# Kernel tuning notes

Measured on AMD Instinct MI355X. Metric: run time of the kernel, lower is better.

The kernel has to match this reference:

```python
import jax, jax.numpy as jnp
import numpy as np

B, N, C, H = 16, 512, 128, 8
T, DEG = B * N, 32
E = T * DEG
EQ = 8            # mul of 0e and of 1o in output irreps
EQD = EQ + 3 * EQ # 32 = irreps_out.dim
RW = 64           # radial MLP width
AVG_NEIGH = 10.0


def setup_inputs() -> dict:
    key = jax.random.key(0)
    ks = jax.random.split(key, 24)
    X = jax.random.normal(ks[0], (B, N, C), jnp.float32)
    adj_mask = jnp.ones((B, H, N, N), bool)
    edge_index = jax.random.randint(ks[1], (2, E), 0, T)
    edge_vectors = jax.random.normal(ks[2], (E, 3), jnp.float32)
    batch_mapping = jnp.repeat(jnp.arange(B), N)  # uniform, sorted
    nrm = lambda k, s, fan: jax.random.normal(k, s, jnp.float32) / np.sqrt(fan)
    p = dict(
        # SAB (set-transformer MAB(X,X)) params
        Wq=nrm(ks[3], (C, C), C), bq=jnp.zeros((C,)),
        Wk=nrm(ks[4], (C, C), C), bk=jnp.zeros((C,)),
        Wv=nrm(ks[5], (C, C), C), bv=jnp.zeros((C,)),
        Wf=nrm(ks[6], (C, C), C), bf=jnp.zeros((C,)),
        g0=jnp.ones((C,)), b0=jnp.zeros((C,)),
        g1=jnp.ones((C,)), b1=jnp.zeros((C,)),
        # cross connection inv->equiv (nn.Linear)
        Wc=nrm(ks[7], (C, C), C), bc=jnp.zeros((C,)),
        # e3nn-style weights (std-1; fan-in normalization applied in forward)
        W1=jax.random.normal(ks[8], (C, C), jnp.float32),        # linear_1 on 0e feats
        Wr0=jax.random.normal(ks[9], (1, RW), jnp.float32),      # radial MLP
        Wr1=jax.random.normal(ks[10], (RW, RW), jnp.float32),
        Wr2=jax.random.normal(ks[11], (RW, 2 * C), jnp.float32),  # 2 tp paths x C channels
        W20=jax.random.normal(ks[12], (C, EQ), jnp.float32),     # linear_2, 0e block
        W21=jax.random.normal(ks[13], (C, EQ), jnp.float32),     # linear_2, 1o block
        Wsc=jax.random.normal(ks[14], (C, EQ), jnp.float32),     # self-connection (0e only)
        # equiv->scalar and gate (nn.Linear on irreps_out.dim=32)
        Wes=nrm(ks[15], (EQD, C), EQD), bes=jnp.zeros((C,)),
        Wg=nrm(ks[16], (EQD, C), EQD), bg=jnp.zeros((C,)),
    )
    return dict(X=X, adj_mask=adj_mask, edge_index=edge_index,
                edge_vectors=edge_vectors, batch_mapping=batch_mapping, **p)


def _ln(x, g, b):
    mu = jnp.mean(x, -1, keepdims=True)
    var = jnp.var(x, -1, keepdims=True)
    return (x - mu) * jax.lax.rsqrt(var + 1e-5) * g + b


def _sab(X, adj_mask, Wq, bq, Wk, bk, Wv, bv, Wf, bf, g0, b0, g1, b1):
    b, n, d = X.shape
    dh = d // H
    q = (X @ Wq + bq).reshape(b, n, H, dh).transpose(0, 2, 1, 3)
    k = (X @ Wk + bk).reshape(b, n, H, dh).transpose(0, 2, 1, 3)
    v = (X @ Wv + bv).reshape(b, n, H, dh).transpose(0, 2, 1, 3)
    s = jnp.einsum('bhqd,bhkd->bhqk', q, k) / np.sqrt(dh)
    s = jnp.where(adj_mask, s, jnp.float32(-1e9))
    a = jax.nn.softmax(s, -1)
    o = q + jnp.einsum('bhqk,bhkd->bhqd', a, v)
    o = o.transpose(0, 2, 1, 3).reshape(b, n, d)
    o = _ln(o, g0, b0)
    o = o + jax.nn.relu(o @ Wf + bf)
    return _ln(o, g1, b1)


def _dense_sparse_idx(batch_mapping):
    counts = jax.ops.segment_sum(jnp.ones_like(batch_mapping), batch_mapping, B)
    offs = jnp.concatenate([jnp.zeros((1,), counts.dtype), jnp.cumsum(counts)[:-1]])
    pos = jnp.arange(batch_mapping.shape[0]) - offs[batch_mapping]
    return pos


def reference(X, adj_mask, edge_index, edge_vectors, batch_mapping,
              Wq, bq, Wk, bk, Wv, bv, Wf, bf, g0, b0, g1, b1,
              Wc, bc, W1, Wr0, Wr1, Wr2, W20, W21, Wsc, Wes, bes, Wg, bg):
    inv = _sab(X, adj_mask, Wq, bq, Wk, bk, Wv, bv, Wf, bf, g0, b0, g1, b1)

    pos = _dense_sparse_idx(batch_mapping)
    x_sp = X[batch_mapping, pos]                         # [T,C] dense->sparse
    xe = x_sp @ Wc + bc                                  # inv_to_equiv
    x1 = xe @ W1 / np.sqrt(C)                            # linear_1 (0e)

    # spherical harmonics (normalize=True, component norm); e3nn order (y,z,x)
    r = edge_vectors / jnp.clip(jnp.linalg.norm(edge_vectors, axis=-1, keepdims=True), 1e-12)
    Y1 = np.sqrt(3.0) * r[:, jnp.array([1, 2, 0])]       # [E,3]; Y0 == 1

    # radial MLP on edge_embedding == 1 (FullyConnectedNet, silu, fan-in norm)
    emb = jnp.ones((edge_index.shape[1], 1), X.dtype)
    h = jax.nn.silu(emb @ Wr0)
    h = jax.nn.silu(h @ Wr1 / np.sqrt(RW))
    w = h @ Wr2 / np.sqrt(RW)                            # [E, 2C]
    w0, w1 = w[:, :C], w[:, C:]

    snd, rcv = edge_index[0], edge_index[1]
    xs = x1[snd]                                         # gather [E,C]
    m0 = w0 * xs                                         # 0e x 0e -> 0e (Y0 = 1)
    m1 = (w1 * xs)[:, :, None] * Y1[:, None, :]          # 0e x 1o -> 1o [E,C,3]
    inv_sqrt = 1.0 / np.sqrt(AVG_NEIGH)
    a0 = jax.ops.segment_sum(m0, rcv, T) * inv_sqrt      # scatter-sum [T,C]
    a1 = jax.ops.segment_sum(m1.reshape(-1, C * 3), rcv, T).reshape(T, C, 3) * inv_sqrt

    out0 = a0 @ W20 / np.sqrt(C)                         # linear_2 per irrep
    out1 = jnp.einsum('tcm,ck->tkm', a1, W21) / np.sqrt(C)
    out0 = out0 + x_sp @ Wsc / np.sqrt(C)                # self-connection (node_attrs=1)
    eq = jnp.concatenate([out0, out1.reshape(T, 3 * EQ)], -1)  # [T,32]

    eq_scalar = eq @ Wes + bes
    gate = eq @ Wg + bg
    eq_dense = jnp.zeros_like(inv).at[batch_mapping, pos].set(eq_scalar)
    gate_dense = jnp.zeros_like(inv).at[batch_mapping, pos].set(gate)

    inv = inv * jax.nn.sigmoid(gate_dense)
    return inv + eq_dense
```

## Files before the change

kernel.cpp:

```cpp
#include <hip/hip_runtime.h>
#include <hip/hip_bf16.h>

#define BB 16
#define NN 512
#define CC 128
#define HH 8
#define DHD 16
#define TT 8192
#define EE 262144
#define RWD 64

__global__ void k_diag(float* __restrict__ out, int n, float code)
{
    int i = blockIdx.x*256 + threadIdx.x;
    if (i < n) out[i] = (i == 0) ? code : 0.f;
}

__global__ __launch_bounds__(512) void k_qkv(const float* __restrict__ X,
    const float* __restrict__ Wq, const float* __restrict__ bq,
    const float* __restrict__ Wk, const float* __restrict__ bk,
    const float* __restrict__ Wv, const float* __restrict__ bv,
    float* __restrict__ qb, float* __restrict__ kb, float* __restrict__ vb,
    int* __restrict__ counts)
{
    __shared__ float a_lds[128][17];
    const int tid  = threadIdx.x;
    const int row0 = blockIdx.x * 16;

    {
        int gid = blockIdx.x*512 + tid;
        if (gid < TT/4) ((int4*)counts)[gid] = make_int4(0,0,0,0);
    }

    const float4* X4 = (const float4*)(X + (size_t)row0*128);
    {
        int r = tid >> 5, k4 = (tid & 31) << 2;
        float4 v = X4[(r*128 + k4) >> 2];
        a_lds[k4+0][r] = v.x; a_lds[k4+1][r] = v.y;
        a_lds[k4+2][r] = v.z; a_lds[k4+3][r] = v.w;
    }
    __syncthreads();

    const int c  = tid & 127;
    const int q4 = tid >> 7;
    const float* Ws[3]  = {Wq, Wk, Wv};
    const float* bsx[3] = {bq, bk, bv};
    float* outs[3] = {qb, kb, vb};

    #pragma unroll
    for (int m = 0; m < 3; m++) {
        float acc[4];
        #pragma unroll
        for (int i = 0; i < 4; i++) acc[i] = 0.f;
        const float* bp = Ws[m] + c;
        for (int k = 0; k < 128; k++) {
            float b = bp[k*128];
            const float* ap = &a_lds[k][q4*4];
            #pragma unroll
            for (int i = 0; i < 4; i++) acc[i] = fmaf(ap[i], b, acc[i]);
        }
        float bia = bsx[m][c];
        float* op = outs[m];
        #pragma unroll
        for (int i = 0; i < 4; i++) {
            int r = row0 + q4*4 + i;
            int b_ = r >> 9, n_ = r & 511, h_ = c >> 4, d_ = c & 15;
            op[(((size_t)(b_*HH + h_)*NN + n_)*DHD) + d_] = acc[i] + bia;
        }
    }
}

__global__ __launch_bounds__(512) void k_attn(const float* __restrict__ qb,
                                              const float* __restrict__ kb,
                                              const float* __restrict__ vb,
                                              float* __restrict__ attn)
{
    __shared__ float k_lds[8192];
    __shared__ float v_lds[8192];
    int bh   = blockIdx.x >> 2;
    int tile = blockIdx.x & 3;
    const float4* kp = (const float4*)(kb + (size_t)bh*8192);
    const float4* vp = (const float4*)(vb + (size_t)bh*8192);
    float4* kl4 = (float4*)k_lds;
    float4* vl4 = (float4*)v_lds;
    for (int i = threadIdx.x; i < 2048; i += 512) {
        float4 kv = kp[i];
        kv.x *= 0.25f; kv.y *= 0.25f; kv.z *= 0.25f; kv.w *= 0.25f;
        kl4[i] = kv;
        vl4[i] = vp[i];
    }

    int r  = threadIdx.x & 127;
    int jq = threadIdx.x >> 7;
    int n  = tile*128 + r;
    float q[16];
    const float4* qp = (const float4*)(qb + ((size_t)bh*512 + n)*16);
    #pragma unroll
    for (int i = 0; i < 4; i++) {
        float4 v = qp[i];
        q[i*4+0] = v.x; q[i*4+1] = v.y; q[i*4+2] = v.z; q[i*4+3] = v.w;
    }
    __syncthreads();

    float l = 0.f, o[16];
    #pragma unroll
    for (int d = 0; d < 16; d++) o[d] = 0.f;

    int j0base = jq*128;
    for (int j0 = j0base; j0 < j0base + 128; j0 += 16) {
        float s[16];
        #pragma unroll
        for (int jj = 0; jj < 16; jj++) {
            const float* kr = &k_lds[(j0 + jj)*16];
            float a = 0.f;
            #pragma unroll
            for (int d = 0; d < 16; d++) a = fmaf(q[d], kr[d], a);
            s[jj] = a;
        }
        #pragma unroll
        for (int jj = 0; jj < 16; jj++) {
            float p = __expf(s[jj]);
            l += p;
            const float* vr = &v_lds[(j0 + jj)*16];
            #pragma unroll
            for (int d = 0; d < 16; d++) o[d] = fmaf(p, vr[d], o[d]);
        }
    }
    __syncthreads();
    float* scr = k_lds;
    if (jq > 0) {
        int base = ((jq-1)*128 + r)*18;
        scr[base + 0] = l;
        #pragma unroll
        for (int d = 0; d < 16; d++) scr[base + 1 + d] = o[d];
    }
    __syncthreads();
    if (jq == 0) {
        const float* s1 = &scr[((size_t)0*128 + r)*18];
        const float* s2 = &scr[((size_t)1*128 + r)*18];
        const float* s3 = &scr[((size_t)2*128 + r)*18];
        float L = l + s1[0] + s2[0] + s3[0];
        float invl = 1.f / L;
        int b_ = bh >> 3, h_ = bh & 7;
        float4* op = (float4*)(attn + ((size_t)(b_*512 + n))*128 + h_*16);
        #pragma unroll
        for (int i = 0; i < 4; i++) {
            float4 v;
            v.x = q[i*4+0] + (o[i*4+0] + s1[1+i*4+0] + s2[1+i*4+0] + s3[1+i*4+0])*invl;
            v.y = q[i*4+1] + (o[i*4+1] + s1[1+i*4+1] + s2[1+i*4+1] + s3[1+i*4+1])*invl;
            v.z = q[i*4+2] + (o[i*4+2] + s1[1+i*4+2] + s2[1+i*4+2] + s3[1+i*4+2])*invl;
            v.w = q[i*4+3] + (o[i*4+3] + s1[1+i*4+3] + s2[1+i*4+3] + s3[1+i*4+3])*invl;
            op[i] = v;
        }
    }
}

__global__ __launch_bounds__(512) void k_ffln(const float* __restrict__ A,
                                              const float* __restrict__ g0,
                                              const float* __restrict__ b0,
                                              const float* __restrict__ Wf,
                                              const float* __restrict__ bfp,
                                              const float* __restrict__ g1,
                                              const float* __restrict__ b1,
                                              float* __restrict__ out)
{
    __shared__ float a_lds[128][36];
    __shared__ float y_lds[32][129];
    __shared__ float red[32][16][2];
    __shared__ float mu_s[32], rs_s[32];
    const int tid  = threadIdx.x;
    const int row0 = blockIdx.x * 32;

    const float4* A4 = (const float4*)(A + (size_t)row0*128);
    for (int fid = tid; fid < 1024; fid += 512) {
        int r = fid >> 5, k4 = (fid & 31) << 2;
        float4 v = A4[(r*128 + k4) >> 2];
        a_lds[k4+0][r] = v.x; a_lds[k4+1][r] = v.y;
        a_lds[k4+2][r] = v.z; a_lds[k4+3][r] = v.w;
    }
    __syncthreads();

    int rr = tid >> 4, seg = tid & 15;
    {
        float s1 = 0.f, s2 = 0.f;
        #pragma unroll
        for (int i = 0; i < 8; i++) {
            float v = a_lds[seg*8 + i][rr];
            s1 += v; s2 += v*v;
        }
        red[rr][seg][0] = s1; red[rr][seg][1] = s2;
    }
    __syncthreads();
    if (seg == 0) {
        float a1 = 0.f, a2 = 0.f;
        #pragma unroll
        for (int s = 0; s < 16; s++) { a1 += red[rr][s][0]; a2 += red[rr][s][1]; }
        float mu = a1 * (1.f/128.f);
        float var = fmaxf(a2 * (1.f/128.f) - mu*mu, 0.f);
        mu_s[rr] = mu; rs_s[rr] = rsqrtf(var + 1e-5f);
    }
    __syncthreads();
    {
        float mu = mu_s[rr], rs = rs_s[rr];
        #pragma unroll
        for (int i = 0; i < 8; i++) {
            int k = seg*8 + i;
            float v = a_lds[k][rr];
            a_lds[k][rr] = (v - mu)*rs*g0[k] + b0[k];
        }
    }
    __syncthreads();

    const int c  = tid & 127;
    const int q4 = tid >> 7;
    float acc[8];
    #pragma unroll
    for (int i = 0; i < 8; i++) acc[i] = 0.f;
    const float* bp = Wf + c;
    for (int k = 0; k < 128; k++) {
        float b = bp[k*128];
        const float* ap = &a_lds[k][q4*8];
        #pragma unroll
        for (int i = 0; i < 8; i++) acc[i] = fmaf(ap[i], b, acc[i]);
    }
    float bia = bfp[c];
    #pragma unroll
    for (int i = 0; i < 8; i++) {
        int rl = q4*8 + i;
        float oln = a_lds[c][rl];
        y_lds[rl][c] = oln + fmaxf(acc[i] + bia, 0.f);
    }
    __syncthreads();

    {
        float s1 = 0.f, s2 = 0.f;
        #pragma unroll
        for (int i = 0; i < 8; i++) {
            float v = y_lds[rr][seg*8 + i];
            s1 += v; s2 += v*v;
        }
        red[rr][seg][0] = s1; red[rr][seg][1] = s2;
    }
    __syncthreads();
    if (seg == 0) {
        float a1 = 0.f, a2 = 0.f;
        #pragma unroll
        for (int s = 0; s < 16; s++) { a1 += red[rr][s][0]; a2 += red[rr][s][1]; }
        float mu = a1 * (1.f/128.f);
        float var = fmaxf(a2 * (1.f/128.f) - mu*mu, 0.f);
        mu_s[rr] = mu; rs_s[rr] = rsqrtf(var + 1e-5f);
    }
    __syncthreads();
    float g = g1[c], bb = b1[c];
    #pragma unroll
    for (int i = 0; i < 8; i++) {
        int rl = q4*8 + i;
        float v = y_lds[rl][c];
        out[(size_t)(row0 + rl)*128 + c] = (v - mu_s[rl])*rs_s[rl]*g + bb;
    }
}

__global__ __launch_bounds__(256) void k_zeq(const float* __restrict__ X,
    const float* __restrict__ Wr0, const float* __restrict__ Wr1,
    const float* __restrict__ Wr2,
    const float* __restrict__ Wc,  const float* __restrict__ W1,
    const float* __restrict__ bc,
    const float* __restrict__ W20, const float* __restrict__ W21,
    const float* __restrict__ Wsc,
    float* __restrict__ z, float* __restrict__ eqsc)
{
    const float SCALE_Z = 0.027950849718747372f;
    const float SC      = 0.08838834764831845f;
    __shared__ float a_lds[128][36];
    __shared__ float w_lds[128*24];
    __shared__ float wz[128][16];
    __shared__ float Pl[128][16];
    __shared__ float wsm[256];
    __shared__ float h0[RWD], h1[RWD];
    __shared__ float be[24];
    int tid = threadIdx.x;
    int row0 = blockIdx.x * 32;

    const float4* X4 = (const float4*)(X + (size_t)row0*128);
    for (int fid = tid; fid < 1024; fid += 256) {
        int r = fid >> 5, k4 = (fid & 31) << 2;
        float4 v = X4[(r*128 + k4) >> 2];
        a_lds[k4+0][r] = v.x; a_lds[k4+1][r] = v.y;
        a_lds[k4+2][r] = v.z; a_lds[k4+3][r] = v.w;
    }
    if (tid < RWD) { float x = Wr0[tid]; h0[tid] = x / (1.f + __expf(-x)); }
    __syncthreads();
    if (tid < RWD) {
        float s = 0.f;
        for (int i = 0; i < RWD; i++) s += h0[i] * Wr1[i*RWD + tid];
        s *= 0.125f;
        h1[tid] = s / (1.f + __expf(-s));
    }
    __syncthreads();
    {
        float s = 0.f;
        for (int i = 0; i < RWD; i++) s += h1[i] * Wr2[i*2*CC + tid];
        wsm[tid] = s * 0.125f;
    }
    __syncthreads();
    for (int idx = tid; idx < 2048; idx += 256) {
        int c = idx >> 4, j = idx & 15;
        wz[c][j] = (j < 8) ? W20[c*8 + j]*wsm[c] : W21[c*8 + (j-8)]*wsm[128 + c];
    }
    __syncthreads();
    {
        int d = tid >> 1, hf = tid & 1;
        float acc[8];
        #pragma unroll
        for (int jj = 0; jj < 8; jj++) acc[jj] = 0.f;
        const float4* wrow = (const float4*)(W1 + (size_t)d*128);
        for (int c4 = 0; c4 < 32; c4++) {
            float4 wv = wrow[c4];
            const float* z0 = &wz[c4*4 + 0][hf*8];
            const float* z1 = &wz[c4*4 + 1][hf*8];
            const float* z2 = &wz[c4*4 + 2][hf*8];
            const float* z3 = &wz[c4*4 + 3][hf*8];
            #pragma unroll
            for (int jj = 0; jj < 8; jj++) {
                float a = acc[jj];
                a = fmaf(wv.x, z0[jj], a);
                a = fmaf(wv.y, z1[jj], a);
                a = fmaf(wv.z, z2[jj], a);
                a = fmaf(wv.w, z3[jj], a);
                acc[jj] = a;
            }
        }
        #pragma unroll
        for (int jj = 0; jj < 8; jj++) Pl[d][hf*8 + jj] = acc[jj];
    }
    __syncthreads();
    {
        int i = tid >> 1, hf = tid & 1;
        float acc[8];
        #pragma unroll
        for (int jj = 0; jj < 8; jj++) acc[jj] = 0.f;
        const float4* crow = (const float4*)(Wc + (size_t)i*128);
        for (int d4 = 0; d4 < 32; d4++) {
            float4 wv = crow[d4];
            const float* p0 = &Pl[d4*4 + 0][hf*8];
            const float* p1 = &Pl[d4*4 + 1][hf*8];
            const float* p2 = &Pl[d4*4 + 2][hf*8];
            const float* p3 = &Pl[d4*4 + 3][hf*8];
            #pragma unroll
            for (int jj = 0; jj < 8; jj++) {
                float a = acc[jj];
                a = fmaf(wv.x, p0[jj], a);
                a = fmaf(wv.y, p1[jj], a);
                a = fmaf(wv.z, p2[jj], a);
                a = fmaf(wv.w, p3[jj], a);
                acc[jj] = a;
            }
        }
        const float SCZ = SC*SCALE_Z;
        #pragma unroll
        for (int jj = 0; jj < 8; jj++) w_lds[i*24 + hf*8 + jj] = acc[jj]*SCZ;
    }
    for (int idx = tid; idx < 1024; idx += 256) {
        int i = idx >> 3, j = idx & 7;
        w_lds[i*24 + 16 + j] = Wsc[i*8 + j]*SC;
    }
    if (tid < 24) {
        float a = 0.f;
        if (tid < 16) {
            for (int d = 0; d < 128; d++) a = fmaf(bc[d], Pl[d][tid], a);
            a *= SC*SCALE_Z;
        }
        be[tid] = a;
    }
    __syncthreads();

    int r = tid >> 3, seg = tid & 7;
    float a0 = be[seg], a1 = be[seg+8], a2 = 0.f;
    for (int k = 0; k < 128; k++) {
        float xv = a_lds[k][r];
        a0 = fmaf(xv, w_lds[k*24 + seg],      a0);
        a1 = fmaf(xv, w_lds[k*24 + seg + 8],  a1);
        a2 = fmaf(xv, w_lds[k*24 + seg + 16], a2);
    }
    size_t t = row0 + r;
    z[t*16 + seg]     = a0;
    z[t*16 + seg + 8] = a1;
    eqsc[t*8 + seg]   = a2;
}

__global__ void k_edge(const int* __restrict__ ei, const float* __restrict__ ev,
                       int* __restrict__ counts, int2* __restrict__ bucket,
                       float* __restrict__ y1)
{
    int e = blockIdx.x*256 + threadIdx.x;
    float x = ev[e*3], y = ev[e*3+1], zz = ev[e*3+2];
    float nrm = sqrtf(x*x + y*y + zz*zz);
    float inv = 1.f / fmaxf(nrm, 1e-12f);
    const float s3 = 1.7320508075688772f;
    y1[e*3 + 0] = s3 * y  * inv;
    y1[e*3 + 1] = s3 * zz * inv;
    y1[e*3 + 2] = s3 * x  * inv;
    int s = ei[e]      & (TT-1);
    int t = ei[EE + e] & (TT-1);
    int pos = atomicAdd(&counts[t], 1);
    if (pos < 128) bucket[(size_t)t*128 + pos] = make_int2(s, e);
}

__global__ __launch_bounds__(256) void k_gfin(const int* __restrict__ counts,
                                              const int2* __restrict__ bucket,
                                              const float* __restrict__ z,
                                              const float* __restrict__ y1,
                                              const float* __restrict__ eqsc,
                                              const float* __restrict__ inv,
                                              const float* __restrict__ Wes,
                                              const float* __restrict__ bes,
                                              const float* __restrict__ Wg,
                                              const float* __restrict__ bg,
                                              float* __restrict__ out)
{
    __shared__ float eql[8][33];
    int tid = threadIdx.x;
    int tb  = blockIdx.x*8;
    int tg  = tid >> 5;
    int t   = tb + tg;
    int j   = tid & 31;
    int deg = counts[t]; if (deg > 128) deg = 128; if (deg < 0) deg = 0;
    const int2* bk = bucket + (size_t)t*128;
    int jj = j - 8;
    int kk = jj / 3;
    int mm = jj - kk*3;
    int zi = (j < 8) ? j : (8 + kk);
    int mi = (j < 8) ? 0 : mm;
    bool isz = (j < 8);

    float ac0 = isz ? eqsc[(size_t)t*8 + j] : 0.f;
    float ac1 = 0.f, ac2 = 0.f, ac3 = 0.f;
    int p = 0;
    for (; p + 8 <= deg; p += 8) {
        int2 e0 = bk[p+0], e1 = bk[p+1], e2 = bk[p+2], e3 = bk[p+3];
        int2 e4 = bk[p+4], e5 = bk[p+5], e6 = bk[p+6], e7 = bk[p+7];
        float z0 = z[(size_t)e0.x*16 + zi], w0 = y1[(size_t)e0.y*3 + mi];
        float z1 = z[(size_t)e1.x*16 + zi], w1 = y1[(size_t)e1.y*3 + mi];
        float z2 = z[(size_t)e2.x*16 + zi], w2 = y1[(size_t)e2.y*3 + mi];
        float z3 = z[(size_t)e3.x*16 + zi], w3 = y1[(size_t)e3.y*3 + mi];
        float z4 = z[(size_t)e4.x*16 + zi], w4 = y1[(size_t)e4.y*3 + mi];
        float z5 = z[(size_t)e5.x*16 + zi], w5 = y1[(size_t)e5.y*3 + mi];
        float z6 = z[(size_t)e6.x*16 + zi], w6 = y1[(size_t)e6.y*3 + mi];
        float z7 = z[(size_t)e7.x*16 + zi], w7 = y1[(size_t)e7.y*3 + mi];
        ac0 = fmaf(z0, isz ? 1.f : w0, ac0);
        ac1 = fmaf(z1, isz ? 1.f : w1, ac1);
        ac2 = fmaf(z2, isz ? 1.f : w2, ac2);
        ac3 = fmaf(z3, isz ? 1.f : w3, ac3);
        ac0 = fmaf(z4, isz ? 1.f : w4, ac0);
        ac1 = fmaf(z5, isz ? 1.f : w5, ac1);
        ac2 = fmaf(z6, isz ? 1.f : w6, ac2);
        ac3 = fmaf(z7, isz ? 1.f : w7, ac3);
    }
    for (; p < deg; p++) {
        int2 se = bk[p];
        float v  = z[(size_t)se.x*16 + zi];
        float wv = y1[(size_t)se.y*3 + mi];
        ac0 = fmaf(v, isz ? 1.f : wv, ac0);
    }
    eql[tg][j] = (ac0 + ac1) + (ac2 + ac3);
    __syncthreads();

    int c = tid & 127, hf = tid >> 7;
    float aes[4], ag[4];
    float bse = bes[c], bgg = bg[c];
    #pragma unroll
    for (int r2 = 0; r2 < 4; r2++) { aes[r2] = bse; ag[r2] = bgg; }
    for (int jx = 0; jx < 32; jx++) {
        float we = Wes[jx*128 + c];
        float wg = Wg [jx*128 + c];
        #pragma unroll
        for (int r2 = 0; r2 < 4; r2++) {
            float v = eql[hf*4 + r2][jx];
            aes[r2] = fmaf(v, we, aes[r2]);
            ag[r2]  = fmaf(v, wg, ag[r2]);
        }
    }
    #pragma unroll
    for (int r2 = 0; r2 < 4; r2++) {
        size_t row = (size_t)tb + hf*4 + r2;
        float g = 1.f / (1.f + __expf(-ag[r2]));
        out[row*128 + c] = inv[row*128 + c] * g + aes[r2];
    }
}

extern "C" void kernel_launch(void* const* d_in, const int* in_sizes, int n_in,
                              void* d_out, int out_size, void* d_ws, size_t ws_size,
                              hipStream_t stream)
{
    int p = 1;
    while (p < n_in && in_sizes[p] != 2*EE) p++;
    if (p >= n_in) p = 2;

    const size_t M = (size_t)TT*CC;
    const size_t NEED_WORDS = 4*M + (size_t)TT*16 + (size_t)TT*32 + 256
                              + 16384 + 128 + 3072 + 32 + TT
                              + (size_t)2*TT*128;
    if (ws_size < NEED_WORDS*4) {
        float code = 1000.f + (float)(ws_size >> 20);
        k_diag<<<(out_size + 255)/256, 256, 0, stream>>>((float*)d_out, out_size, code);
        return;
    }

    const float* X   = (const float*)d_in[0];
    const int*   ei  = (const int*)  d_in[p];
    const float* ev  = (const float*)d_in[p+1];
    const int wb = p + 3;
    const float* Wq  = (const float*)d_in[wb+0];  const float* bq = (const float*)d_in[wb+1];
    const float* Wk  = (const float*)d_in[wb+2];  const float* bk = (const float*)d_in[wb+3];
    const float* Wv  = (const float*)d_in[wb+4];  const float* bv = (const float*)d_in[wb+5];
    const float* Wf  = (const float*)d_in[wb+6];  const float* bf_= (const float*)d_in[wb+7];
    const float* g0  = (const float*)d_in[wb+8];  const float* b0 = (const float*)d_in[wb+9];
    const float* g1  = (const float*)d_in[wb+10]; const float* b1 = (const float*)d_in[wb+11];
    const float* Wc  = (const float*)d_in[wb+12]; const float* bc = (const float*)d_in[wb+13];
    const float* W1  = (const float*)d_in[wb+14];
    const float* Wr0 = (const float*)d_in[wb+15];
    const float* Wr1 = (const float*)d_in[wb+16];
    const float* Wr2 = (const float*)d_in[wb+17];
    const float* W20 = (const float*)d_in[wb+18];
    const float* W21 = (const float*)d_in[wb+19];
    const float* Wsc = (const float*)d_in[wb+20];
    const float* Wes = (const float*)d_in[wb+21]; const float* bes = (const float*)d_in[wb+22];
    const float* Wg  = (const float*)d_in[wb+23]; const float* bg  = (const float*)d_in[wb+24];

    float* ws   = (float*)d_ws;
    float* A_   = ws;
    float* B_   = ws + M;
    float* C_   = ws + 2*M;
    float* D_   = ws + 3*M;
    float* z    = ws + 4*M;
    float* eqsc = z + (size_t)TT*16;
    float* w    = eqsc + (size_t)TT*32;
    float* Wcc  = w + 256;
    float* bcc  = Wcc + 16384;
    float* W24  = bcc + 128;
    float* beff = W24 + 3072;
    int*   counts = (int*)(beff + 32);
    int2*  bucket = (int2*)(counts + TT);
    float* y1     = B_;

    k_qkv<<<TT/16, 512, 0, stream>>>(X, Wq, bq, Wk, bk, Wv, bv, A_, B_, C_, counts);
    k_attn<<<BB*HH*4, 512, 0, stream>>>(A_, B_, C_, D_);
    k_ffln<<<TT/32, 512, 0, stream>>>(D_, g0, b0, Wf, bf_, g1, b1, D_);

    k_zeq<<<TT/32, 256, 0, stream>>>(X, Wr0, Wr1, Wr2, Wc, W1, bc,
                                     W20, W21, Wsc, z, eqsc);

    k_edge<<<EE/256, 256, 0, stream>>>(ei, ev, counts, bucket, y1);
    k_gfin<<<TT/8, 256, 0, stream>>>(counts, bucket, z, y1, eqsc, D_,
                                     Wes, bes, Wg, bg, (float*)d_out);
}
```

Before: 366.8 us.

## Merge QKV with zeq into one kernel and fold edge preprocessing into attention

QKV projection and the zeq node precompute now run as one horizontally fused launch, with blocks split by index and shared memory overlaid through a union. The edge preprocessing (spherical harmonics, atomic bucketing) moves into the attention kernel, one edge per thread across its 512x512 threads. The edge output y1 gets its own workspace region because it previously aliased the K buffer. This removes two launches and lets independent work overlap, at the cost of a larger shared-memory footprint per block and extra global work inside attention before its barrier.

```diff
diff --git a/kernel.cpp b/kernel.cpp
--- a/kernel.cpp
+++ b/kernel.cpp
@@ -16,64 +16,202 @@
     if (i < n) out[i] = (i == 0) ? code : 0.f;
 }
 
-__global__ __launch_bounds__(512) void k_qkv(const float* __restrict__ X,
+struct ZeqSm {
+    float a_lds[128][36];
+    float w_lds[128*24];
+    float wz[128][16];
+    float Pl[128][16];
+    float wsm[256];
+    float h0[RWD], h1[RWD];
+    float be[24];
+};
+union MegaSm {
+    float qkv_a[128][17];
+    ZeqSm z;
+};
+
+__global__ __launch_bounds__(512) void k_mega1(const float* __restrict__ X,
     const float* __restrict__ Wq, const float* __restrict__ bq,
     const float* __restrict__ Wk, const float* __restrict__ bk,
     const float* __restrict__ Wv, const float* __restrict__ bv,
+    const float* __restrict__ Wr0, const float* __restrict__ Wr1,
+    const float* __restrict__ Wr2,
+    const float* __restrict__ Wc,  const float* __restrict__ W1,
+    const float* __restrict__ bc,
+    const float* __restrict__ W20, const float* __restrict__ W21,
+    const float* __restrict__ Wsc,
     float* __restrict__ qb, float* __restrict__ kb, float* __restrict__ vb,
+    float* __restrict__ z, float* __restrict__ eqsc,
     int* __restrict__ counts)
 {
-    __shared__ float a_lds[128][17];
-    const int tid  = threadIdx.x;
-    const int row0 = blockIdx.x * 16;
-
-    {
-        int gid = blockIdx.x*512 + tid;
-        if (gid < TT/4) ((int4*)counts)[gid] = make_int4(0,0,0,0);
-    }
-
-    const float4* X4 = (const float4*)(X + (size_t)row0*128);
-    {
-        int r = tid >> 5, k4 = (tid & 31) << 2;
-        float4 v = X4[(r*128 + k4) >> 2];
-        a_lds[k4+0][r] = v.x; a_lds[k4+1][r] = v.y;
-        a_lds[k4+2][r] = v.z; a_lds[k4+3][r] = v.w;
-    }
-    __syncthreads();
-
-    const int c  = tid & 127;
-    const int q4 = tid >> 7;
-    const float* Ws[3]  = {Wq, Wk, Wv};
-    const float* bsx[3] = {bq, bk, bv};
-    float* outs[3] = {qb, kb, vb};
-
-    #pragma unroll
-    for (int m = 0; m < 3; m++) {
-        float acc[4];
-        #pragma unroll
-        for (int i = 0; i < 4; i++) acc[i] = 0.f;
-        const float* bp = Ws[m] + c;
+    __shared__ MegaSm sm;
+    const int tid = threadIdx.x;
+
+    if (blockIdx.x < 512) {
+        const int row0 = blockIdx.x * 16;
+        {
+            int gid = blockIdx.x*512 + tid;
+            if (gid < TT/4) ((int4*)counts)[gid] = make_int4(0,0,0,0);
+        }
+        const float4* X4 = (const float4*)(X + (size_t)row0*128);
+        {
+            int r = tid >> 5, k4 = (tid & 31) << 2;
+            float4 v = X4[(r*128 + k4) >> 2];
+            sm.qkv_a[k4+0][r] = v.x; sm.qkv_a[k4+1][r] = v.y;
+            sm.qkv_a[k4+2][r] = v.z; sm.qkv_a[k4+3][r] = v.w;
+        }
+        __syncthreads();
+
+        const int c  = tid & 127;
+        const int q4 = tid >> 7;
+        const float* Ws[3]  = {Wq, Wk, Wv};
+        const float* bsx[3] = {bq, bk, bv};
+        float* outs[3] = {qb, kb, vb};
+
+        #pragma unroll
+        for (int m = 0; m < 3; m++) {
+            float acc[4];
+            #pragma unroll
+            for (int i = 0; i < 4; i++) acc[i] = 0.f;
+            const float* bp = Ws[m] + c;
+            for (int k = 0; k < 128; k++) {
+                float b = bp[k*128];
+                const float* ap = &sm.qkv_a[k][q4*4];
+                #pragma unroll
+                for (int i = 0; i < 4; i++) acc[i] = fmaf(ap[i], b, acc[i]);
+            }
+            float bia = bsx[m][c];
+            float* op = outs[m];
+            #pragma unroll
+            for (int i = 0; i < 4; i++) {
+                int r = row0 + q4*4 + i;
+                int b_ = r >> 9, n_ = r & 511, h_ = c >> 4, d_ = c & 15;
+                op[(((size_t)(b_*HH + h_)*NN + n_)*DHD) + d_] = acc[i] + bia;
+            }
+        }
+    } else {
+        const float SCALE_Z = 0.027950849718747372f;
+        const float SC      = 0.08838834764831845f;
+        ZeqSm& S = sm.z;
+        const int row0 = (blockIdx.x - 512) * 32;
+
+        const float4* X4 = (const float4*)(X + (size_t)row0*128);
+        for (int fid = tid; fid < 1024; fid += 512) {
+            int r = fid >> 5, k4 = (fid & 31) << 2;
+            float4 v = X4[(r*128 + k4) >> 2];
+            S.a_lds[k4+0][r] = v.x; S.a_lds[k4+1][r] = v.y;
+            S.a_lds[k4+2][r] = v.z; S.a_lds[k4+3][r] = v.w;
+        }
+        if (tid < RWD) { float x = Wr0[tid]; S.h0[tid] = x / (1.f + __expf(-x)); }
+        __syncthreads();
+        if (tid < RWD) {
+            float s = 0.f;
+            for (int i = 0; i < RWD; i++) s += S.h0[i] * Wr1[i*RWD + tid];
+            s *= 0.125f;
+            S.h1[tid] = s / (1.f + __expf(-s));
+        }
+        __syncthreads();
+        if (tid < 256) {
+            float s = 0.f;
+            for (int i = 0; i < RWD; i++) s += S.h1[i] * Wr2[i*2*CC + tid];
+            S.wsm[tid] = s * 0.125f;
+        }
+        __syncthreads();
+        for (int idx = tid; idx < 2048; idx += 512) {
+            int c = idx >> 4, j = idx & 15;
+            S.wz[c][j] = (j < 8) ? W20[c*8 + j]*S.wsm[c]
+                                 : W21[c*8 + (j-8)]*S.wsm[128 + c];
+        }
+        __syncthreads();
+        {
+            int d = tid >> 2, qf = tid & 3;
+            float acc[4];
+            #pragma unroll
+            for (int jj = 0; jj < 4; jj++) acc[jj] = 0.f;
+            const float4* wrow = (const float4*)(W1 + (size_t)d*128);
+            for (int c4 = 0; c4 < 32; c4++) {
+                float4 wv = wrow[c4];
+                const float* z0 = &S.wz[c4*4 + 0][qf*4];
+                const float* z1 = &S.wz[c4*4 + 1][qf*4];
+                const float* z2 = &S.wz[c4*4 + 2][qf*4];
+                const float* z3 = &S.wz[c4*4 + 3][qf*4];
+                #pragma unroll
+                for (int jj = 0; jj < 4; jj++) {
+                    float a = acc[jj];
+                    a = fmaf(wv.x, z0[jj], a);
+                    a = fmaf(wv.y, z1[jj], a);
+                    a = fmaf(wv.z, z2[jj], a);
+                    a = fmaf(wv.w, z3[jj], a);
+                    acc[jj] = a;
+                }
+            }
+            #pragma unroll
+            for (int jj = 0; jj < 4; jj++) S.Pl[d][qf*4 + jj] = acc[jj];
+        }
+        __syncthreads();
+        {
+            int i = tid >> 2, qf = tid & 3;
+            float acc[4];
+            #pragma unroll
+            for (int jj = 0; jj < 4; jj++) acc[jj] = 0.f;
+            const float4* crow = (const float4*)(Wc + (size_t)i*128);
+            for (int d4 = 0; d4 < 32; d4++) {
+                float4 wv = crow[d4];
+                const float* p0 = &S.Pl[d4*4 + 0][qf*4];
+                const float* p1 = &S.Pl[d4*4 + 1][qf*4];
+                const float* p2 = &S.Pl[d4*4 + 2][qf*4];
+                const float* p3 = &S.Pl[d4*4 + 3][qf*4];
+                #pragma unroll
+                for (int jj = 0; jj < 4; jj++) {
+                    float a = acc[jj];
+                    a = fmaf(wv.x, p0[jj], a);
+                    a = fmaf(wv.y, p1[jj], a);
+                    a = fmaf(wv.z, p2[jj], a);
+                    a = fmaf(wv.w, p3[jj], a);
+                    acc[jj] = a;
+                }
+            }
+            const float SCZ = SC*SCALE_Z;
+            #pragma unroll
+            for (int jj = 0; jj < 4; jj++) S.w_lds[i*24 + qf*4 + jj] = acc[jj]*SCZ;
+        }
+        for (int idx = tid; idx < 1024; idx += 512) {
+            int i = idx >> 3, j = idx & 7;
+            S.w_lds[i*24 + 16 + j] = Wsc[i*8 + j]*SC;
+        }
+        if (tid < 24) {
+            float a = 0.f;
+            if (tid < 16) {
+                for (int d = 0; d < 128; d++) a = fmaf(bc[d], S.Pl[d][tid], a);
+                a *= SC*SCALE_Z;
+            }
+            S.be[tid] = a;
+        }
+        __syncthreads();
+
+        int r = tid >> 4, sg = tid & 15;
+        int sg2 = sg & 7;
+        float a = S.be[sg], a2 = 0.f;
         for (int k = 0; k < 128; k++) {
-            float b = bp[k*128];
-            const float* ap = &a_lds[k][q4*4];
-            #pragma unroll
-            for (int i = 0; i < 4; i++) acc[i] = fmaf(ap[i], b, acc[i]);
-        }
-        float bia = bsx[m][c];
-        float* op = outs[m];
-        #pragma unroll
-        for (int i = 0; i < 4; i++) {
-            int r = row0 + q4*4 + i;
-            int b_ = r >> 9, n_ = r & 511, h_ = c >> 4, d_ = c & 15;
-            op[(((size_t)(b_*HH + h_)*NN + n_)*DHD) + d_] = acc[i] + bia;
-        }
+            float xv = S.a_lds[k][r];
+            a  = fmaf(xv, S.w_lds[k*24 + sg], a);
+            a2 = fmaf(xv, S.w_lds[k*24 + 16 + sg2], a2);
+        }
+        size_t t = row0 + r;
+        z[t*16 + sg] = a;
+        if (sg < 8) eqsc[t*8 + sg] = a2;
     }
 }
 
-__global__ __launch_bounds__(512) void k_attn(const float* __restrict__ qb,
-                                              const float* __restrict__ kb,
-                                              const float* __restrict__ vb,
-                                              float* __restrict__ attn)
+__global__ __launch_bounds__(512) void k_attn_edge(const float* __restrict__ qb,
+                                                   const float* __restrict__ kb,
+                                                   const float* __restrict__ vb,
+                                                   const int* __restrict__ ei,
+                                                   const float* __restrict__ ev,
+                                                   int* __restrict__ counts,
+                                                   int2* __restrict__ bucket,
+                                                   float* __restrict__ y1,
+                                                   float* __restrict__ attn)
 {
     __shared__ float k_lds[8192];
     __shared__ float v_lds[8192];
@@ -99,6 +237,21 @@
     for (int i = 0; i < 4; i++) {
         float4 v = qp[i];
         q[i*4+0] = v.x; q[i*4+1] = v.y; q[i*4+2] = v.z; q[i*4+3] = v.w;
+    }
+
+    {
+        int e = blockIdx.x*512 + threadIdx.x;
+        float x = ev[e*3], y = ev[e*3+1], zz = ev[e*3+2];
+        float nrm = sqrtf(x*x + y*y + zz*zz);
+        float inv = 1.f / fmaxf(nrm, 1e-12f);
+        const float s3 = 1.7320508075688772f;
+        y1[e*3 + 0] = s3 * y  * inv;
+        y1[e*3 + 1] = s3 * zz * inv;
+        y1[e*3 + 2] = s3 * x  * inv;
+        int s = ei[e]      & (TT-1);
+        int t = ei[EE + e] & (TT-1);
+        int pos = atomicAdd(&counts[t], 1);
+        if (pos < 128) bucket[(size_t)t*128 + pos] = make_int2(s, e);
     }
     __syncthreads();
 
@@ -258,152 +411,6 @@
         float v = y_lds[rl][c];
         out[(size_t)(row0 + rl)*128 + c] = (v - mu_s[rl])*rs_s[rl]*g + bb;
     }
-}
-
-__global__ __launch_bounds__(256) void k_zeq(const float* __restrict__ X,
-    const float* __restrict__ Wr0, const float* __restrict__ Wr1,
-    const float* __restrict__ Wr2,
-    const float* __restrict__ Wc,  const float* __restrict__ W1,
-    const float* __restrict__ bc,
-    const float* __restrict__ W20, const float* __restrict__ W21,
-    const float* __restrict__ Wsc,
-    float* __restrict__ z, float* __restrict__ eqsc)
-{
-    const float SCALE_Z = 0.027950849718747372f;
-    const float SC      = 0.08838834764831845f;
-    __shared__ float a_lds[128][36];
-    __shared__ float w_lds[128*24];
-    __shared__ float wz[128][16];
-    __shared__ float Pl[128][16];
-    __shared__ float wsm[256];
-    __shared__ float h0[RWD], h1[RWD];
-    __shared__ float be[24];
-    int tid = threadIdx.x;
-    int row0 = blockIdx.x * 32;
-
-    const float4* X4 = (const float4*)(X + (size_t)row0*128);
-    for (int fid = tid; fid < 1024; fid += 256) {
-        int r = fid >> 5, k4 = (fid & 31) << 2;
-        float4 v = X4[(r*128 + k4) >> 2];
-        a_lds[k4+0][r] = v.x; a_lds[k4+1][r] = v.y;
-        a_lds[k4+2][r] = v.z; a_lds[k4+3][r] = v.w;
-    }
-    if (tid < RWD) { float x = Wr0[tid]; h0[tid] = x / (1.f + __expf(-x)); }
-    __syncthreads();
-    if (tid < RWD) {
-        float s = 0.f;
-        for (int i = 0; i < RWD; i++) s += h0[i] * Wr1[i*RWD + tid];
-        s *= 0.125f;
-        h1[tid] = s / (1.f + __expf(-s));
-    }
-    __syncthreads();
-    {
-        float s = 0.f;
-        for (int i = 0; i < RWD; i++) s += h1[i] * Wr2[i*2*CC + tid];
-        wsm[tid] = s * 0.125f;
-    }
-    __syncthreads();
-    for (int idx = tid; idx < 2048; idx += 256) {
-        int c = idx >> 4, j = idx & 15;
-        wz[c][j] = (j < 8) ? W20[c*8 + j]*wsm[c] : W21[c*8 + (j-8)]*wsm[128 + c];
-    }
-    __syncthreads();
-    {
-        int d = tid >> 1, hf = tid & 1;
-        float acc[8];
-        #pragma unroll
-        for (int jj = 0; jj < 8; jj++) acc[jj] = 0.f;
-        const float4* wrow = (const float4*)(W1 + (size_t)d*128);
-        for (int c4 = 0; c4 < 32; c4++) {
-            float4 wv = wrow[c4];
-            const float* z0 = &wz[c4*4 + 0][hf*8];
-            const float* z1 = &wz[c4*4 + 1][hf*8];
-            const float* z2 = &wz[c4*4 + 2][hf*8];
-            const float* z3 = &wz[c4*4 + 3][hf*8];
-            #pragma unroll
-            for (int jj = 0; jj < 8; jj++) {
-                float a = acc[jj];
-                a = fmaf(wv.x, z0[jj], a);
-                a = fmaf(wv.y, z1[jj], a);
-                a = fmaf(wv.z, z2[jj], a);
-                a = fmaf(wv.w, z3[jj], a);
-                acc[jj] = a;
-            }
-        }
-        #pragma unroll
-        for (int jj = 0; jj < 8; jj++) Pl[d][hf*8 + jj] = acc[jj];
-    }
-    __syncthreads();
-    {
-        int i = tid >> 1, hf = tid & 1;
-        float acc[8];
-        #pragma unroll
-        for (int jj = 0; jj < 8; jj++) acc[jj] = 0.f;
-        const float4* crow = (const float4*)(Wc + (size_t)i*128);
-        for (int d4 = 0; d4 < 32; d4++) {
-            float4 wv = crow[d4];
-            const float* p0 = &Pl[d4*4 + 0][hf*8];
-            const float* p1 = &Pl[d4*4 + 1][hf*8];
-            const float* p2 = &Pl[d4*4 + 2][hf*8];
-            const float* p3 = &Pl[d4*4 + 3][hf*8];
-            #pragma unroll
-            for (int jj = 0; jj < 8; jj++) {
-                float a = acc[jj];
-                a = fmaf(wv.x, p0[jj], a);
-                a = fmaf(wv.y, p1[jj], a);
-                a = fmaf(wv.z, p2[jj], a);
-                a = fmaf(wv.w, p3[jj], a);
-                acc[jj] = a;
-            }
-        }
-        const float SCZ = SC*SCALE_Z;
-        #pragma unroll
-        for (int jj = 0; jj < 8; jj++) w_lds[i*24 + hf*8 + jj] = acc[jj]*SCZ;
-    }
-    for (int idx = tid; idx < 1024; idx += 256) {
-        int i = idx >> 3, j = idx & 7;
-        w_lds[i*24 + 16 + j] = Wsc[i*8 + j]*SC;
-    }
-    if (tid < 24) {
-        float a = 0.f;
-        if (tid < 16) {
-            for (int d = 0; d < 128; d++) a = fmaf(bc[d], Pl[d][tid], a);
-            a *= SC*SCALE_Z;
-        }
-        be[tid] = a;
-    }
-    __syncthreads();
-
-    int r = tid >> 3, seg = tid & 7;
-    float a0 = be[seg], a1 = be[seg+8], a2 = 0.f;
-    for (int k = 0; k < 128; k++) {
-        float xv = a_lds[k][r];
-        a0 = fmaf(xv, w_lds[k*24 + seg],      a0);
-        a1 = fmaf(xv, w_lds[k*24 + seg + 8],  a1);
-        a2 = fmaf(xv, w_lds[k*24 + seg + 16], a2);
-    }
-    size_t t = row0 + r;
-    z[t*16 + seg]     = a0;
-    z[t*16 + seg + 8] = a1;
-    eqsc[t*8 + seg]   = a2;
-}
-
-__global__ void k_edge(const int* __restrict__ ei, const float* __restrict__ ev,
-                       int* __restrict__ counts, int2* __restrict__ bucket,
-                       float* __restrict__ y1)
-{
-    int e = blockIdx.x*256 + threadIdx.x;
-    float x = ev[e*3], y = ev[e*3+1], zz = ev[e*3+2];
-    float nrm = sqrtf(x*x + y*y + zz*zz);
-    float inv = 1.f / fmaxf(nrm, 1e-12f);
-    const float s3 = 1.7320508075688772f;
-    y1[e*3 + 0] = s3 * y  * inv;
-    y1[e*3 + 1] = s3 * zz * inv;
-    y1[e*3 + 2] = s3 * x  * inv;
-    int s = ei[e]      & (TT-1);
-    int t = ei[EE + e] & (TT-1);
-    int pos = atomicAdd(&counts[t], 1);
-    if (pos < 128) bucket[(size_t)t*128 + pos] = make_int2(s, e);
 }
 
 __global__ __launch_bounds__(256) void k_gfin(const int* __restrict__ counts,
@@ -499,7 +506,8 @@
     const size_t M = (size_t)TT*CC;
     const size_t NEED_WORDS = 4*M + (size_t)TT*16 + (size_t)TT*32 + 256
                               + 16384 + 128 + 3072 + 32 + TT
-                              + (size_t)2*TT*128;
+                              + (size_t)2*TT*128
+                              + (size_t)3*EE;
     if (ws_size < NEED_WORDS*4) {
         float code = 1000.f + (float)(ws_size >> 20);
         k_diag<<<(out_size + 255)/256, 256, 0, stream>>>((float*)d_out, out_size, code);
@@ -541,16 +549,17 @@
     float* beff = W24 + 3072;
     int*   counts = (int*)(beff + 32);
     int2*  bucket = (int2*)(counts + TT);
-    float* y1     = B_;
-
-    k_qkv<<<TT/16, 512, 0, stream>>>(X, Wq, bq, Wk, bk, Wv, bv, A_, B_, C_, counts);
-    k_attn<<<BB*HH*4, 512, 0, stream>>>(A_, B_, C_, D_);
+    float* y1     = (float*)(bucket + (size_t)TT*128);
+
+    k_mega1<<<768, 512, 0, stream>>>(X, Wq, bq, Wk, bk, Wv, bv,
+                                     Wr0, Wr1, Wr2, Wc, W1, bc, W20, W21, Wsc,
+                                     A_, B_, C_, z, eqsc, counts);
+
+    k_attn_edge<<<BB*HH*4, 512, 0, stream>>>(A_, B_, C_, ei, ev,
+                                             counts, bucket, y1, D_);
+
     k_ffln<<<TT/32, 512, 0, stream>>>(D_, g0, b0, Wf, bf_, g1, b1, D_);
 
-    k_zeq<<<TT/32, 256, 0, stream>>>(X, Wr0, Wr1, Wr2, Wc, W1, bc,
-                                     W20, W21, Wsc, z, eqsc);
-
-    k_edge<<<EE/256, 256, 0, stream>>>(ei, ev, counts, bucket, y1);
     k_gfin<<<TT/8, 256, 0, stream>>>(counts, bucket, z, y1, eqsc, D_,
                                      Wes, bes, Wg, bg, (float*)d_out);
 }
```

Measured after the change: 349.0 us. 1.05x faster.
